# Optimization experiments

Measured on AMD Instinct MI355X. Metric: run time of the kernel, lower is better.

Reference implementation:

```python
import jax, jax.numpy as jnp
import numpy as np

C1 = 256
C2 = 256
C = 256

def setup_inputs() -> dict:
    key = jax.random.key(0)
    ks = jax.random.split(key, 8)
    B, S, H, W = 4, 8, 32, 32
    img_feat = jax.random.normal(ks[0], (B, S, C1, H, W), dtype=jnp.float32)
    depth_feat = jax.random.normal(ks[1], (B, S, C2, H, W), dtype=jnp.float32)
    sq = 1.0 / np.sqrt(C1)
    sk = 1.0 / np.sqrt(C2)
    Wq = jax.random.uniform(ks[2], (C1, C), jnp.float32, -sq, sq)
    bq = jax.random.uniform(ks[3], (C,), jnp.float32, -sq, sq)
    Wk = jax.random.uniform(ks[4], (C2, C), jnp.float32, -sk, sk)
    bk = jax.random.uniform(ks[5], (C,), jnp.float32, -sk, sk)
    Wv = jax.random.uniform(ks[6], (C2, C), jnp.float32, -sk, sk)
    bv = jax.random.uniform(ks[7], (C,), jnp.float32, -sk, sk)
    return {"img_feat": img_feat, "depth_feat": depth_feat,
            "Wq": Wq, "bq": bq, "Wk": Wk, "bk": bk, "Wv": Wv, "bv": bv}

def reference(img_feat, depth_feat, Wq, bq, Wk, bk, Wv, bv):
    B, S, _, H, W = img_feat.shape
    hw = H * W
    # channels-last, flatten spatial: [B,S,hw,c1]
    img = jnp.transpose(img_feat, (0, 1, 3, 4, 2)).reshape(B, S, hw, -1)
    depth = jnp.transpose(depth_feat, (0, 1, 3, 4, 2)).reshape(B, S, hw, -1)
    q = (img @ Wq + bq).astype(jnp.float32)    # [B,S,hw,c]
    k = (depth @ Wk + bk).astype(jnp.float32)  # [B,S,hw,c]
    v = (depth @ Wv + bv).astype(jnp.float32)  # [B,S,hw,c]
    scale = 1.0 / jnp.sqrt(jnp.float32(Wq.shape[1]))
    scores = jnp.einsum('bsqc,bskc->bsqk', q, k) * scale  # [B,S,hw,hw]
    attn = jax.nn.softmax(scores, axis=-1)
    out = jnp.einsum('bsqk,bskc->bsqc', attn, v)          # [B,S,hw,c]
    out = out + img                                        # residual (c == c1)
    out = out.reshape(B, S, H, W, -1).astype(img_feat.dtype)
    return jnp.transpose(out, (0, 1, 4, 2, 3))             # [B,S,c,H,W]
```

## Files before the change

### kernel.cpp

```cpp
#include <hip/hip_runtime.h>
#include <hip/hip_bf16.h>

typedef __hip_bfloat16 bf16;
typedef __attribute__((ext_vector_type(8))) short short8v;
typedef __attribute__((ext_vector_type(4))) float f32x4;

#define NSLICE 32
#define HW     1024
#define CDIM   256
#define KVT    32

__global__ __launch_bounds__(256)
void wt_prep_kernel(const float* __restrict__ Wq, const float* __restrict__ Wk,
                    const float* __restrict__ Wv, bf16* __restrict__ wt)
{
    const int m = blockIdx.x >> 8;
    const int r = blockIdx.x & 255;
    const int tid = threadIdx.x;
    const float* W = (m == 0) ? Wq : (m == 1) ? Wk : Wv;
    const float sc = (m == 0) ? 0.0625f : 1.0f;
    wt[((size_t)m << 16) + (size_t)tid * 256 + r] = __float2bfloat16(W[r * 256 + tid] * sc);
}

__global__ __launch_bounds__(256)
void proj_q_kernel(const float* __restrict__ img, const bf16* __restrict__ wt,
                   const float* __restrict__ bq, bf16* __restrict__ qo)
{
    const int bid   = blockIdx.x;
    const int s     = (bid & 7) * 4 + ((bid >> 3) & 3);
    const int tt    = (bid >> 5) & 15;
    const int chalf = bid >> 9;
    const int t0    = tt * 64;

    const int tid  = threadIdx.x;
    const int wave = tid >> 6;
    const int lane = tid & 63;
    const int lo16 = lane & 15;
    const int hi4  = lane >> 4;
    const int cw0  = chalf * 128 + wave * 32;

    __shared__ short Ai[64][40];

    const int so = tid >> 6, st = tid & 63;
    const float* imgS = img + (size_t)s * CDIM * HW + t0;

    f32x4 aq[2][4];
    #pragma unroll
    for (int a = 0; a < 2; ++a)
        #pragma unroll
        for (int b = 0; b < 4; ++b) aq[a][b] = (f32x4){0.f, 0.f, 0.f, 0.f};

    float ri[8];
    #pragma unroll
    for (int j = 0; j < 8; ++j) ri[j] = imgS[(size_t)(so * 8 + j) * HW + st];

    for (int kc = 0; kc < 8; ++kc) {
        __syncthreads();
        {
            short ti[8];
            #pragma unroll
            for (int j = 0; j < 8; ++j) {
                bf16 hb = __float2bfloat16(ri[j]);
                ti[j] = *reinterpret_cast<short*>(&hb);
            }
            *reinterpret_cast<short8v*>(&Ai[st][so * 8]) = *reinterpret_cast<short8v*>(ti);
        }
        __syncthreads();

        if (kc < 7) {
            #pragma unroll
            for (int j = 0; j < 8; ++j)
                ri[j] = imgS[(size_t)((kc + 1) * 32 + so * 8 + j) * HW + st];
        }

        short8v xi[4];
        #pragma unroll
        for (int nf = 0; nf < 4; ++nf)
            xi[nf] = *reinterpret_cast<const short8v*>(&Ai[nf * 16 + lo16][hi4 * 8]);

        const int koff = kc * 32 + hi4 * 8;
        short8v wqf[2];
        #pragma unroll
        for (int mf = 0; mf < 2; ++mf)
            wqf[mf] = *reinterpret_cast<const short8v*>(
                wt + (size_t)(cw0 + mf * 16 + lo16) * 256 + koff);

        #pragma unroll
        for (int mf = 0; mf < 2; ++mf)
            #pragma unroll
            for (int nf = 0; nf < 4; ++nf)
                aq[mf][nf] = __builtin_amdgcn_mfma_f32_16x16x32_bf16(wqf[mf], xi[nf], aq[mf][nf], 0, 0, 0);
    }

    #pragma unroll
    for (int mf = 0; mf < 2; ++mf) {
        const int cb = cw0 + mf * 16 + 4 * hi4;
        const float4 b4 = *reinterpret_cast<const float4*>(bq + cb);
        const float ba[4] = {b4.x * 0.0625f, b4.y * 0.0625f, b4.z * 0.0625f, b4.w * 0.0625f};
        #pragma unroll
        for (int nf = 0; nf < 4; ++nf) {
            const int tok = t0 + nf * 16 + lo16;
            bf16 tq[4];
            #pragma unroll
            for (int g = 0; g < 4; ++g)
                tq[g] = __float2bfloat16(aq[mf][nf][g] + ba[g]);
            *reinterpret_cast<uint2*>(&qo[((size_t)s * HW + tok) * CDIM + cb]) =
                *reinterpret_cast<uint2*>(tq);
        }
    }
}

__global__ __launch_bounds__(256)
void proj_kv_kernel(const float* __restrict__ dep, const bf16* __restrict__ wt,
                    const float* __restrict__ bk, const float* __restrict__ bv,
                    bf16* __restrict__ ko, bf16* __restrict__ vt)
{
    const int bid   = blockIdx.x;
    const int s     = (bid & 7) * 4 + ((bid >> 3) & 3);
    const int tt    = (bid >> 5) & 15;
    const int chalf = bid >> 9;
    const int t0    = tt * 64;

    const int tid  = threadIdx.x;
    const int wave = tid >> 6;
    const int lane = tid & 63;
    const int lo16 = lane & 15;
    const int hi4  = lane >> 4;
    const int cw0  = chalf * 128 + wave * 32;

    __shared__ short Ad[64][40];

    const int so = tid >> 6, st = tid & 63;
    const float* depS = dep + (size_t)s * CDIM * HW + t0;
    const bf16* wtk = wt + (1 << 16);
    const bf16* wtv = wt + (2 << 16);

    f32x4 ak[2][4], av[4][2];
    #pragma unroll
    for (int a = 0; a < 2; ++a)
        #pragma unroll
        for (int b = 0; b < 4; ++b) {
            ak[a][b] = (f32x4){0.f, 0.f, 0.f, 0.f};
            av[b][a] = (f32x4){0.f, 0.f, 0.f, 0.f};
        }

    float rd[8];
    #pragma unroll
    for (int j = 0; j < 8; ++j) rd[j] = depS[(size_t)(so * 8 + j) * HW + st];

    for (int kc = 0; kc < 8; ++kc) {
        __syncthreads();
        {
            short td[8];
            #pragma unroll
            for (int j = 0; j < 8; ++j) {
                bf16 hb = __float2bfloat16(rd[j]);
                td[j] = *reinterpret_cast<short*>(&hb);
            }
            *reinterpret_cast<short8v*>(&Ad[st][so * 8]) = *reinterpret_cast<short8v*>(td);
        }
        __syncthreads();

        if (kc < 7) {
            #pragma unroll
            for (int j = 0; j < 8; ++j)
                rd[j] = depS[(size_t)((kc + 1) * 32 + so * 8 + j) * HW + st];
        }

        short8v xd[4];
        #pragma unroll
        for (int nf = 0; nf < 4; ++nf)
            xd[nf] = *reinterpret_cast<const short8v*>(&Ad[nf * 16 + lo16][hi4 * 8]);

        const int koff = kc * 32 + hi4 * 8;
        short8v wkf[2], wvf[2];
        #pragma unroll
        for (int mf = 0; mf < 2; ++mf) {
            const size_t wrow = (size_t)(cw0 + mf * 16 + lo16) * 256 + koff;
            wkf[mf] = *reinterpret_cast<const short8v*>(wtk + wrow);
            wvf[mf] = *reinterpret_cast<const short8v*>(wtv + wrow);
        }

        #pragma unroll
        for (int mf = 0; mf < 2; ++mf)
            #pragma unroll
            for (int nf = 0; nf < 4; ++nf)
                ak[mf][nf] = __builtin_amdgcn_mfma_f32_16x16x32_bf16(wkf[mf], xd[nf], ak[mf][nf], 0, 0, 0);
        #pragma unroll
        for (int mf = 0; mf < 4; ++mf)
            #pragma unroll
            for (int nf = 0; nf < 2; ++nf)
                av[mf][nf] = __builtin_amdgcn_mfma_f32_16x16x32_bf16(xd[mf], wvf[nf], av[mf][nf], 0, 0, 0);
    }

    #pragma unroll
    for (int mf = 0; mf < 2; ++mf) {
        const int cb = cw0 + mf * 16 + 4 * hi4;
        const float4 b4 = *reinterpret_cast<const float4*>(bk + cb);
        const float ba[4] = {b4.x, b4.y, b4.z, b4.w};
        #pragma unroll
        for (int nf = 0; nf < 4; ++nf) {
            const int tok = t0 + nf * 16 + lo16;
            bf16 tk[4];
            #pragma unroll
            for (int g = 0; g < 4; ++g)
                tk[g] = __float2bfloat16(ak[mf][nf][g] + ba[g]);
            *reinterpret_cast<uint2*>(&ko[((size_t)s * HW + tok) * CDIM + cb]) =
                *reinterpret_cast<uint2*>(tk);
        }
    }
    #pragma unroll
    for (int nf = 0; nf < 2; ++nf) {
        const int c = cw0 + nf * 16 + lo16;
        const float bvv = bv[c];
        #pragma unroll
        for (int mf = 0; mf < 4; ++mf) {
            const int tb = t0 + mf * 16 + 4 * hi4;
            bf16 tv[4];
            #pragma unroll
            for (int g = 0; g < 4; ++g)
                tv[g] = __float2bfloat16(av[mf][nf][g] + bvv);
            *reinterpret_cast<uint2*>(&vt[((size_t)s * CDIM + c) * HW + tb]) =
                *reinterpret_cast<uint2*>(tv);
        }
    }
}

__global__ __launch_bounds__(256)
void flash_mfma_kernel(const bf16* __restrict__ q, const bf16* __restrict__ k,
                       const bf16* __restrict__ vt, const float* __restrict__ img,
                       float* __restrict__ out)
{
    const int bid = blockIdx.x;
    const int s   = (bid & 7) * 4 + ((bid >> 3) & 3);
    const int t0  = (bid >> 5) * 64;

    const int tid  = threadIdx.x;
    const int wave = tid >> 6;
    const int lane = tid & 63;
    const int lo16 = lane & 15;
    const int hi4  = lane >> 4;

    __shared__ short KsL[32 * 256];
    __shared__ short VsL[256 * 32];
    __shared__ short PsL[4 * 16 * 32];

    short8v qf[8];
    {
        const bf16* qp = q + ((size_t)s * HW + t0 + wave * 16 + lo16) * CDIM + hi4 * 8;
        #pragma unroll
        for (int kf = 0; kf < 8; ++kf)
            qf[kf] = *reinterpret_cast<const short8v*>(qp + kf * 32);
    }

    f32x4 Oacc[16];
    #pragma unroll
    for (int cf = 0; cf < 16; ++cf) Oacc[cf] = (f32x4){0.f, 0.f, 0.f, 0.f};
    float lp[4] = {0.f, 0.f, 0.f, 0.f};

    const bf16* kS  = k  + (size_t)s * HW * CDIM;
    const bf16* vtS = vt + (size_t)s * CDIM * HW;

    const int krow = tid >> 3;
    const int kch  = tid & 7;
    const int kxor = krow & 7;
    const int vxor = (tid >> 1) & 3;

    short8v kreg[4], vreg[4];
    #pragma unroll
    for (int u = 0; u < 4; ++u) {
        kreg[u] = *reinterpret_cast<const short8v*>(kS + (size_t)krow * CDIM + (kch + 8 * u) * 8);
        vreg[u] = *reinterpret_cast<const short8v*>(vtS + (size_t)tid * HW + u * 8);
    }

    const int pvRow = lo16 * 32 + (hi4 ^ ((lo16 >> 1) & 3)) * 8;
    for (int kt = 0; kt < HW / KVT; ++kt) {
        __syncthreads();
        #pragma unroll
        for (int u = 0; u < 4; ++u)
            *reinterpret_cast<short8v*>(&KsL[krow * 256 + ((kch ^ kxor) + 8 * u) * 8]) = kreg[u];
        #pragma unroll
        for (int u = 0; u < 4; ++u)
            *reinterpret_cast<short8v*>(&VsL[tid * 32 + (u ^ vxor) * 8]) = vreg[u];
        __syncthreads();

        if (kt + 1 < HW / KVT) {
            const bf16* src = kS + (size_t)(kt + 1) * KVT * CDIM;
            #pragma unroll
            for (int u = 0; u < 4; ++u) {
                kreg[u] = *reinterpret_cast<const short8v*>(src + (size_t)krow * CDIM + (kch + 8 * u) * 8);
                vreg[u] = *reinterpret_cast<const short8v*>(vtS + (size_t)tid * HW + (kt + 1) * KVT + u * 8);
            }
        }

        f32x4 sa[2];
        sa[0] = (f32x4){0.f, 0.f, 0.f, 0.f};
        sa[1] = (f32x4){0.f, 0.f, 0.f, 0.f};
        __builtin_amdgcn_s_setprio(1);
        #pragma unroll
        for (int ks = 0; ks < 8; ++ks) {
            #pragma unroll
            for (int cf = 0; cf < 2; ++cf) {
                const int row = cf * 16 + lo16;
                short8v bfr = *reinterpret_cast<const short8v*>(
                    &KsL[row * 256 + ((4 * ks + hi4) ^ (lo16 & 7)) * 8]);
                sa[cf] = __builtin_amdgcn_mfma_f32_16x16x32_bf16(qf[ks], bfr, sa[cf], 0, 0, 0);
            }
        }
        __builtin_amdgcn_s_setprio(0);

        #pragma unroll
        for (int cf = 0; cf < 2; ++cf)
            #pragma unroll
            for (int g = 0; g < 4; ++g) {
                const float e = __expf(sa[cf][g]);
                lp[g] += e;
                bf16 hb = __float2bfloat16(e);
                const int r = 4 * hi4 + g;
                const int ch = (2 * cf + (lo16 >> 3)) ^ ((r >> 1) & 3);
                PsL[wave * 512 + r * 32 + ch * 8 + (lo16 & 7)] = *reinterpret_cast<short*>(&hb);
            }

        const short8v pa = *reinterpret_cast<const short8v*>(&PsL[wave * 512 + pvRow]);

        __builtin_amdgcn_s_setprio(1);
        #pragma unroll
        for (int cf = 0; cf < 16; ++cf) {
            const int row = cf * 16 + lo16;
            const short8v vb = *reinterpret_cast<const short8v*>(
                &VsL[row * 32 + (hi4 ^ ((lo16 >> 1) & 3)) * 8]);
            Oacc[cf] = __builtin_amdgcn_mfma_f32_16x16x32_bf16(pa, vb, Oacc[cf], 0, 0, 0);
        }
        __builtin_amdgcn_s_setprio(0);
    }

    float inv[4];
    #pragma unroll
    for (int g = 0; g < 4; ++g) {
        float l = lp[g];
        #pragma unroll
        for (int off = 1; off < 16; off <<= 1) l += __shfl_xor(l, off);
        inv[g] = 1.0f / l;
    }
    const float* imgS = img + (size_t)s * CDIM * HW;
    float*       outS = out + (size_t)s * CDIM * HW;
    const int tt = t0 + wave * 16 + 4 * hi4;
    #pragma unroll
    for (int cf = 0; cf < 16; ++cf) {
        const int c = cf * 16 + lo16;
        const float4 r4 = *reinterpret_cast<const float4*>(imgS + (size_t)c * HW + tt);
        float4 o;
        o.x = Oacc[cf][0] * inv[0] + r4.x;
        o.y = Oacc[cf][1] * inv[1] + r4.y;
        o.z = Oacc[cf][2] * inv[2] + r4.z;
        o.w = Oacc[cf][3] * inv[3] + r4.w;
        *reinterpret_cast<float4*>(outS + (size_t)c * HW + tt) = o;
    }
}

extern "C" void kernel_launch(void* const* d_in, const int* in_sizes, int n_in,
                              void* d_out, int out_size, void* d_ws, size_t ws_size,
                              hipStream_t stream)
{
    const float* img = (const float*)d_in[0];
    const float* dep = (const float*)d_in[1];
    const float* Wq  = (const float*)d_in[2];
    const float* bq  = (const float*)d_in[3];
    const float* Wk  = (const float*)d_in[4];
    const float* bk  = (const float*)d_in[5];
    const float* Wv  = (const float*)d_in[6];
    const float* bv  = (const float*)d_in[7];
    float* out = (float*)d_out;

    const size_t npt  = (size_t)NSLICE * HW * CDIM;
    const size_t need = 3 * npt * sizeof(bf16) + 3 * 65536 * sizeof(bf16);
    if (ws_size < need) {
        hipMemsetAsync(d_out, 0, (size_t)out_size * sizeof(float), stream);
        return;
    }

    bf16* q  = (bf16*)d_ws;
    bf16* k  = q + npt;
    bf16* vt = k + npt;
    bf16* wt = vt + npt;

    wt_prep_kernel<<<dim3(3 * 256), 256, 0, stream>>>(Wq, Wk, Wv, wt);

    proj_q_kernel<<<dim3(NSLICE * 32), 256, 0, stream>>>(img, wt, bq, q);
    proj_kv_kernel<<<dim3(NSLICE * 32), 256, 0, stream>>>(dep, wt, bk, bv, k, vt);

    flash_mfma_kernel<<<dim3(NSLICE * 16), 256, 0, stream>>>(q, k, vt, img, out);
}
```

Before: 123.0 us.

## Double-buffer K/V tiles in LDS to drop one barrier per iteration

Moves the flash kernel's K, V and P staging into one dynamic LDS buffer with two K/V slots. The next tile is written into the alternate slot after the PV MFMAs, so each loop iteration needs one __syncthreads instead of two. LDS use roughly doubles to about 68 KB per block, which may reduce how many blocks fit on a CU. It also adds a hipFuncSetAttribute call on every launch.

```diff
diff --git a/kernel.cpp b/kernel.cpp
--- a/kernel.cpp
+++ b/kernel.cpp
@@ -9,6 +9,9 @@
 #define HW     1024
 #define CDIM   256
 #define KVT    32
+#define NKT    (HW / KVT)
+
+#define FLASH_LDS_BYTES ((32768 + 2048) * 2)
 
 __global__ __launch_bounds__(256)
 void wt_prep_kernel(const float* __restrict__ Wq, const float* __restrict__ Wk,
@@ -241,9 +244,7 @@
     const int lo16 = lane & 15;
     const int hi4  = lane >> 4;
 
-    __shared__ short KsL[32 * 256];
-    __shared__ short VsL[256 * 32];
-    __shared__ short PsL[4 * 16 * 32];
+    extern __shared__ short SM[];
 
     short8v qf[8];
     {
@@ -273,18 +274,22 @@
         vreg[u] = *reinterpret_cast<const short8v*>(vtS + (size_t)tid * HW + u * 8);
     }
 
+    #pragma unroll
+    for (int u = 0; u < 4; ++u)
+        *reinterpret_cast<short8v*>(&SM[krow * 256 + ((kch ^ kxor) + 8 * u) * 8]) = kreg[u];
+    #pragma unroll
+    for (int u = 0; u < 4; ++u)
+        *reinterpret_cast<short8v*>(&SM[16384 + tid * 32 + (u ^ vxor) * 8]) = vreg[u];
+    __syncthreads();
+
     const int pvRow = lo16 * 32 + (hi4 ^ ((lo16 >> 1) & 3)) * 8;
-    for (int kt = 0; kt < HW / KVT; ++kt) {
-        __syncthreads();
-        #pragma unroll
-        for (int u = 0; u < 4; ++u)
-            *reinterpret_cast<short8v*>(&KsL[krow * 256 + ((kch ^ kxor) + 8 * u) * 8]) = kreg[u];
-        #pragma unroll
-        for (int u = 0; u < 4; ++u)
-            *reinterpret_cast<short8v*>(&VsL[tid * 32 + (u ^ vxor) * 8]) = vreg[u];
-        __syncthreads();
-
-        if (kt + 1 < HW / KVT) {
+    for (int kt = 0; kt < NKT; ++kt) {
+        const int cur = kt & 1;
+        const int nxt = cur ^ 1;
+        short* Kc = SM + cur * 8192;
+        short* Vc = SM + 16384 + cur * 8192;
+
+        if (kt + 1 < NKT) {
             const bf16* src = kS + (size_t)(kt + 1) * KVT * CDIM;
             #pragma unroll
             for (int u = 0; u < 4; ++u) {
@@ -303,7 +308,7 @@
             for (int cf = 0; cf < 2; ++cf) {
                 const int row = cf * 16 + lo16;
                 short8v bfr = *reinterpret_cast<const short8v*>(
-                    &KsL[row * 256 + ((4 * ks + hi4) ^ (lo16 & 7)) * 8]);
+                    &Kc[row * 256 + ((4 * ks + hi4) ^ (lo16 & 7)) * 8]);
                 sa[cf] = __builtin_amdgcn_mfma_f32_16x16x32_bf16(qf[ks], bfr, sa[cf], 0, 0, 0);
             }
         }
@@ -318,20 +323,32 @@
                 bf16 hb = __float2bfloat16(e);
                 const int r = 4 * hi4 + g;
                 const int ch = (2 * cf + (lo16 >> 3)) ^ ((r >> 1) & 3);
-                PsL[wave * 512 + r * 32 + ch * 8 + (lo16 & 7)] = *reinterpret_cast<short*>(&hb);
+                SM[32768 + wave * 512 + r * 32 + ch * 8 + (lo16 & 7)] = *reinterpret_cast<short*>(&hb);
             }
 
-        const short8v pa = *reinterpret_cast<const short8v*>(&PsL[wave * 512 + pvRow]);
+        const short8v pa = *reinterpret_cast<const short8v*>(&SM[32768 + wave * 512 + pvRow]);
 
         __builtin_amdgcn_s_setprio(1);
         #pragma unroll
         for (int cf = 0; cf < 16; ++cf) {
             const int row = cf * 16 + lo16;
             const short8v vb = *reinterpret_cast<const short8v*>(
-                &VsL[row * 32 + (hi4 ^ ((lo16 >> 1) & 3)) * 8]);
+                &Vc[row * 32 + (hi4 ^ ((lo16 >> 1) & 3)) * 8]);
             Oacc[cf] = __builtin_amdgcn_mfma_f32_16x16x32_bf16(pa, vb, Oacc[cf], 0, 0, 0);
         }
         __builtin_amdgcn_s_setprio(0);
+
+        if (kt + 1 < NKT) {
+            short* Kn = SM + nxt * 8192;
+            short* Vn = SM + 16384 + nxt * 8192;
+            #pragma unroll
+            for (int u = 0; u < 4; ++u)
+                *reinterpret_cast<short8v*>(&Kn[krow * 256 + ((kch ^ kxor) + 8 * u) * 8]) = kreg[u];
+            #pragma unroll
+            for (int u = 0; u < 4; ++u)
+                *reinterpret_cast<short8v*>(&Vn[tid * 32 + (u ^ vxor) * 8]) = vreg[u];
+        }
+        __syncthreads();
     }
 
     float inv[4];
@@ -384,10 +401,15 @@
     bf16* vt = k + npt;
     bf16* wt = vt + npt;
 
+    hipFuncSetAttribute((const void*)flash_mfma_kernel,
+                        hipFuncAttributeMaxDynamicSharedMemorySize,
+                        FLASH_LDS_BYTES);
+
     wt_prep_kernel<<<dim3(3 * 256), 256, 0, stream>>>(Wq, Wk, Wv, wt);
 
     proj_q_kernel<<<dim3(NSLICE * 32), 256, 0, stream>>>(img, wt, bq, q);
     proj_kv_kernel<<<dim3(NSLICE * 32), 256, 0, stream>>>(dep, wt, bk, bv, k, vt);
 
-    flash_mfma_kernel<<<dim3(NSLICE * 16), 256, 0, stream>>>(q, k, vt, img, out);
+    flash_mfma_kernel<<<dim3(NSLICE * 16), 256, FLASH_LDS_BYTES, stream>>>(
+        q, k, vt, img, out);
 }
```

Result: no change. 122.7 us, median of 3 (-0.2%).
